# Optimization experiments

Hardware: AMD Instinct MI355X
Metric: run time of the kernel (lower is better)

Reference implementation:

```python
import jax, jax.numpy as jnp
import numpy as np
import math

HIDDEN = 2048
N_HEADS = 16
HEAD_DIM = HIDDEN // N_HEADS
BASE = 10000.0


def setup_inputs() -> dict:
    key = jax.random.key(0)
    ks = jax.random.split(key, 8)
    s = 1.0 / math.sqrt(HIDDEN)
    inp = {
        "hidden_states": jax.random.normal(ks[0], (2, 2048, HIDDEN), dtype=jnp.float32),
        "Wq": jax.random.normal(ks[1], (HIDDEN, HIDDEN), dtype=jnp.float32) * s,
        "bq": jax.random.normal(ks[2], (HIDDEN,), dtype=jnp.float32) * s,
        "Wk": jax.random.normal(ks[3], (HIDDEN, HIDDEN), dtype=jnp.float32) * s,
        "bk": jax.random.normal(ks[4], (HIDDEN,), dtype=jnp.float32) * s,
        "Wv": jax.random.normal(ks[5], (HIDDEN, HIDDEN), dtype=jnp.float32) * s,
        "bv": jax.random.normal(ks[6], (HIDDEN,), dtype=jnp.float32) * s,
        "Wo": jax.random.normal(ks[7], (HIDDEN, HIDDEN), dtype=jnp.float32) * s,
    }
    return inp


def _rotate_half(x):
    x1, x2 = x[..., : x.shape[-1] // 2], x[..., x.shape[-1] // 2 :]
    return jnp.concatenate((-x2, x1), axis=-1)


def _rope_cos_sin(seq_len, dtype):
    inv_freq = 1.0 / (BASE ** (jnp.arange(0, HEAD_DIM, 2, dtype=jnp.float32) / HEAD_DIM))
    t = jnp.arange(seq_len, dtype=jnp.float32)
    freqs = jnp.einsum("i,j->ij", t, inv_freq)  # [S, head_dim/2]
    emb = jnp.concatenate((freqs, freqs), axis=-1)  # [S, head_dim]
    return jnp.cos(emb).astype(dtype), jnp.sin(emb).astype(dtype)


def reference(hidden_states, Wq, bq, Wk, bk, Wv, bv, Wo):
    B, S, _ = hidden_states.shape
    q = hidden_states @ Wq + bq
    k = hidden_states @ Wk + bk
    v = hidden_states @ Wv + bv
    # [B, H, S, D]
    q = q.reshape(B, S, N_HEADS, HEAD_DIM).transpose(0, 2, 1, 3)
    k = k.reshape(B, S, N_HEADS, HEAD_DIM).transpose(0, 2, 1, 3)
    v = v.reshape(B, S, N_HEADS, HEAD_DIM).transpose(0, 2, 1, 3)
    cos, sin = _rope_cos_sin(S, q.dtype)  # [S, D]
    cos = cos[None, None]
    sin = sin[None, None]
    q = q * cos + _rotate_half(q) * sin
    k = k * cos + _rotate_half(k) * sin
    scale = 1.0 / math.sqrt(HEAD_DIM)
    scores = jnp.einsum("bhqd,bhkd->bhqk", q, k) * scale
    attn = jax.nn.softmax(scores, axis=-1)
    out = jnp.einsum("bhqk,bhkd->bhqd", attn, v)
    out = out.transpose(0, 2, 1, 3).reshape(B, S, HIDDEN)
    return out @ Wo
```

## Files before the change

kernel.cpp:

```cpp
#include <hip/hip_runtime.h>

#define HID 2048
#define SEQ 2048
#define HD 128
#define QKN 6144

typedef float f32x4 __attribute__((ext_vector_type(4)));
typedef float f32x16 __attribute__((ext_vector_type(16)));
typedef short s16x8 __attribute__((ext_vector_type(8)));
typedef __bf16 bf16x8 __attribute__((ext_vector_type(8)));

static __device__ __forceinline__ unsigned short f2bf(float x) {
    unsigned u = __float_as_uint(x);
    u = u + 0x7FFFu + ((u >> 16) & 1u);
    return (unsigned short)(u >> 16);
}
static __device__ __forceinline__ float bf2f(unsigned short h) {
    return __uint_as_float(((unsigned)h) << 16);
}
static __device__ __forceinline__ bf16x8 as_bf(s16x8 v) {
    union { s16x8 s; bf16x8 b; } u; u.s = v; return u.b;
}
static __device__ __forceinline__ bf16x8 ld_bf8(const unsigned short* p) {
    return as_bf(*(const s16x8*)p);
}
static __device__ __forceinline__ void gload_lds16(const void* g, void* l) {
    __builtin_amdgcn_global_load_lds(
        (const __attribute__((address_space(1))) void*)g,
        (__attribute__((address_space(3))) void*)l,
        16, 0, 0);
}

__global__ __launch_bounds__(256) void fill_f32(
    float* __restrict__ out, float v, int n)
{
    int i = blockIdx.x * 256 + threadIdx.x;
    if (i < n) out[i] = v;
}

__global__ __launch_bounds__(256) void convert_f32_bf16(
    const float* __restrict__ in, unsigned short* __restrict__ out)
{
    long i = ((long)blockIdx.x * 256 + threadIdx.x) * 8;
    f32x4 a = *(const f32x4*)&in[i];
    f32x4 b = *(const f32x4*)&in[i + 4];
    s16x8 o;
#pragma unroll
    for (int e = 0; e < 4; ++e) {
        o[e]     = (short)f2bf(a[e]);
        o[e + 4] = (short)f2bf(b[e]);
    }
    *(s16x8*)&out[i] = o;
}

__global__ __launch_bounds__(256) void transpose_w4(
    const float* __restrict__ Wq, const float* __restrict__ Wk,
    const float* __restrict__ Wv, const float* __restrict__ Wo,
    unsigned short* __restrict__ wqkvT, unsigned short* __restrict__ woT)
{
    __shared__ float t[32][33];
    const int z = blockIdx.z;
    const float* W = (z == 0) ? Wq : (z == 1) ? Wk : (z == 2) ? Wv : Wo;
    unsigned short* Wt = (z < 3) ? (wqkvT + (long)z * HID * HID) : woT;
    int k0 = blockIdx.x * 32, n0 = blockIdx.y * 32;
    int tx = threadIdx.x & 31, ty = threadIdx.x >> 5;
#pragma unroll
    for (int r = ty; r < 32; r += 8)
        t[r][tx] = W[(long)(k0 + r) * HID + n0 + tx];
    __syncthreads();
#pragma unroll
    for (int r = ty; r < 32; r += 8)
        Wt[(long)(n0 + r) * HID + k0 + tx] = f2bf(t[tx][r]);
}

template<int NF, bool F32OUT, bool ROPE>
__global__ __launch_bounds__(512, 2) void gemm_8phase(
    const unsigned short* __restrict__ A,
    const unsigned short* __restrict__ Bt,
    const float* __restrict__ bq, const float* __restrict__ bk,
    const float* __restrict__ bv,
    unsigned short* __restrict__ Cb, float* __restrict__ Cf,
    int K, int ldc, int nbn, int sm, int sn, int hasBias)
{
    constexpr int BUFE = 16384 + NF * 4096;
    __shared__ unsigned short lds[2 * BUFE];
    const int tid = threadIdx.x;
    const int wid = tid >> 6, lane = tid & 63;
    const int l16 = lane & 15, l4 = lane >> 4;
    const int wm = wid >> 2, wn = wid & 3;

    const int bid = blockIdx.x;
    const int xcd = bid & 7, idx = bid >> 3;
    const int ncn = nbn / sn;
    const int cm = xcd / ncn, cn = xcd % ncn;
    const int lm = idx / sn,  ln = idx % sn;
    const long bm = (long)(cm * sm + lm) * 256;
    const long bn = (long)(cn * sn + ln) * (NF * 64);

    const int NT = K >> 6;
    const long strideB = (long)K * 2;
    const int srow = tid >> 3;
    const int scb  = ((tid & 7) * 16) ^ ((srow & 7) << 4);

    auto stageA = [&](int t, int c) {
        unsigned short* base = &lds[(t & 1) * BUFE];
        const int row = c * 64 + srow;
        const char* src = (const char*)A + (bm + row) * strideB + (long)t * 128 + scb;
        gload_lds16(src, base + (c * 64 + wid * 8) * 64);
    };
    auto stageB = [&](int t, int c) {
        unsigned short* base = &lds[(t & 1) * BUFE + 16384];
        const int row = c * 64 + srow;
        const char* src = (const char*)Bt + (bn + row) * strideB + (long)t * 128 + scb;
        gload_lds16(src, base + (c * 64 + wid * 8) * 64);
    };

    f32x4 acc[8][NF];
#pragma unroll
    for (int i = 0; i < 8; ++i)
#pragma unroll
        for (int j = 0; j < NF; ++j) acc[i][j] = f32x4{0.f, 0.f, 0.f, 0.f};

    auto compute = [&](const unsigned short* Ab, const unsigned short* Bb) {
#pragma unroll
        for (int kk = 0; kk < 2; ++kk) {
            bf16x8 bfr[NF];
#pragma unroll
            for (int j = 0; j < NF; ++j) {
                const int row = wn * (NF * 16) + j * 16 + l16;
                const char* rb = (const char*)Bb + row * 128;
                bfr[j] = as_bf(*(const s16x8*)(rb + ((kk * 64 + l4 * 16) ^ ((l16 & 7) << 4))));
            }
#pragma unroll
            for (int half = 0; half < 2; ++half) {
                bf16x8 af[4];
#pragma unroll
                for (int i = 0; i < 4; ++i) {
                    const int row = wm * 128 + (half * 4 + i) * 16 + l16;
                    const char* rb = (const char*)Ab + row * 128;
                    af[i] = as_bf(*(const s16x8*)(rb + ((kk * 64 + l4 * 16) ^ ((l16 & 7) << 4))));
                }
                __builtin_amdgcn_s_setprio(1);
#pragma unroll
                for (int i = 0; i < 4; ++i)
#pragma unroll
                    for (int j = 0; j < NF; ++j)
                        acc[half * 4 + i][j] = __builtin_amdgcn_mfma_f32_16x16x32_bf16(
                            af[i], bfr[j], acc[half * 4 + i][j], 0, 0, 0);
                __builtin_amdgcn_s_setprio(0);
            }
        }
    };

#pragma unroll
    for (int c = 0; c < 4; ++c) stageA(0, c);
#pragma unroll
    for (int c = 0; c < NF; ++c) stageB(0, c);

    for (int t = 0; t < NT - 1; ++t) {
        const unsigned short* Ab = &lds[(t & 1) * BUFE];
        const unsigned short* Bb = Ab + 16384;
#pragma unroll
        for (int c = 0; c < 4; ++c) stageA(t + 1, c);
#pragma unroll
        for (int c = 0; c < NF; ++c) stageB(t + 1, c);
        __builtin_amdgcn_sched_barrier(0);
        if constexpr (NF == 6)      asm volatile("s_waitcnt vmcnt(10)" ::: "memory");
        else if constexpr (NF == 3) asm volatile("s_waitcnt vmcnt(7)" ::: "memory");
        else                        asm volatile("s_waitcnt vmcnt(6)" ::: "memory");
        __builtin_amdgcn_s_barrier();
        __builtin_amdgcn_sched_barrier(0);
        compute(Ab, Bb);
        __builtin_amdgcn_s_barrier();
    }
    {
        const unsigned short* Ab = &lds[((NT - 1) & 1) * BUFE];
        const unsigned short* Bb = Ab + 16384;
        asm volatile("s_waitcnt vmcnt(0)" ::: "memory");
        __builtin_amdgcn_s_barrier();
        __builtin_amdgcn_sched_barrier(0);
        compute(Ab, Bb);
    }

    float bvv[NF];
#pragma unroll
    for (int nf = 0; nf < NF; ++nf) {
        const long n = bn + wn * (NF * 16) + nf * 16 + l16;
        bvv[nf] = 0.f;
        if (hasBias)
            bvv[nf] = (n < HID) ? bq[n] : ((n < 2 * HID) ? bk[n - HID] : bv[n - 2 * HID]);
    }

    if constexpr (ROPE) {
        constexpr int NH = NF / 2;
        float* fl = (float*)lds;
        const int jr = tid & 63;
        const int rquo = tid >> 6;
        const float inv = exp2f(-(float)jr * 0.20762050593046f);
#pragma unroll
        for (int c = 0; c < 4; ++c) {
            __builtin_amdgcn_s_barrier();
            if (wm == (c >> 1)) {
                const int mf0 = (c & 1) * 4;
#pragma unroll
                for (int mfi = 0; mfi < 4; ++mfi)
#pragma unroll
                    for (int r = 0; r < 4; ++r) {
                        const int rl = mfi * 16 + l4 * 4 + r;
#pragma unroll
                        for (int nf = 0; nf < NF; ++nf)
                            fl[rl * 385 + wn * (NF * 16) + nf * 16 + l16] =
                                acc[mf0 + mfi][nf][r] + bvv[nf];
                    }
            }
            __builtin_amdgcn_s_barrier();
#pragma unroll
            for (int rr = 0; rr < 8; ++rr) {
                const int rl = rr * 8 + rquo;
                const long m = bm + (c >> 1) * 128 + (c & 1) * 64 + rl;
                const int s = (int)(m & (SEQ - 1));
                float sn, cs;
                sincosf((float)s * inv, &sn, &cs);
#pragma unroll
                for (int hh = 0; hh < NH; ++hh) {
                    const long n = bn + hh * 128 + jr;
                    const bool ron = n < 2 * HID;
                    const float qsv = (n < HID) ? 0.12751744581845f : 1.0f;
                    const float se = ron ? sn : 0.f;
                    const float ce = ron ? cs : 1.f;
                    const float x1 = fl[rl * 385 + hh * 128 + jr];
                    const float x2 = fl[rl * 385 + hh * 128 + jr + 64];
                    Cb[m * (long)ldc + n]      = f2bf((x1 * ce - x2 * se) * qsv);
                    Cb[m * (long)ldc + n + 64] = f2bf((x2 * ce + x1 * se) * qsv);
                }
            }
        }
    } else {
#pragma unroll
        for (int mf = 0; mf < 8; ++mf) {
#pragma unroll
            for (int r = 0; r < 4; ++r) {
                const long m = bm + wm * 128 + mf * 16 + l4 * 4 + r;
#pragma unroll
                for (int nf = 0; nf < NF; ++nf) {
                    const long n = bn + wn * (NF * 16) + nf * 16 + l16;
                    float v = acc[mf][nf][r] + bvv[nf];
                    if (F32OUT) Cf[m * (long)ldc + n] = v;
                    else        Cb[m * (long)ldc + n] = f2bf(v);
                }
            }
        }
    }
}

__global__ __launch_bounds__(256) void v_transpose(
    const unsigned short* __restrict__ qkv, unsigned short* __restrict__ vt)
{
    __shared__ unsigned short t[32][33];
    int bh = blockIdx.z;
    int b = bh >> 4, h = bh & 15;
    int s0 = blockIdx.x * 32, d0 = blockIdx.y * 32;
    int tx = threadIdx.x & 31, ty = threadIdx.x >> 5;
#pragma unroll
    for (int r = ty; r < 32; r += 8)
        t[r][tx] = qkv[(long)(b * SEQ + s0 + r) * QKN + 2 * HID + h * HD + d0 + tx];
    __syncthreads();
#pragma unroll
    for (int r = ty; r < 32; r += 8)
        vt[((long)bh * HD + d0 + r) * SEQ + s0 + tx] = t[tx][r];
}

__global__ __launch_bounds__(512, 2) void attn_kernel(
    const unsigned short* __restrict__ qkv,
    const unsigned short* __restrict__ vt,
    unsigned short* __restrict__ attnout)
{
    __shared__ unsigned short Ks[2][64 * 128];
    __shared__ unsigned short Vs[2][128 * 64];

    const int tid = threadIdx.x, wid = tid >> 6, lane = tid & 63;
    const int l32 = lane & 31, hh = lane >> 5;
    const int l16 = lane & 15, l4 = lane >> 4;
    const int bid = blockIdx.x;
    const int xcd = bid & 7, idx = bid >> 3;
    const int bh = xcd * 4 + (idx >> 3);
    const int qt = idx & 7;
    const int b = bh >> 4, h = bh & 15;
    const long rowbase = (long)b * SEQ;

    const unsigned short* Kg = &qkv[rowbase * QKN + HID + h * HD];
    const unsigned short* Vg = &vt[(long)bh * HD * SEQ];

    auto stage = [&](int buf, int kv0) {
#pragma unroll
        for (int i = 0; i < 2; ++i) {
            int c = wid * 2 + i;
            int kr = c * 4 + l4;
            int kcb = (l16 * 16) ^ ((kr & 7) << 4);
            gload_lds16((const char*)(Kg + (long)(kv0 + kr) * QKN) + kcb, &Ks[buf][c * 512]);
            int vr = c * 8 + (lane >> 3);
            int vcb = ((lane & 7) * 16) ^ ((vr & 7) << 4);
            gload_lds16((const char*)(Vg + (long)vr * SEQ + kv0) + vcb, &Vs[buf][c * 512]);
        }
    };

    bf16x8 qf[8];
    {
        const long qrow = rowbase + qt * 256 + wid * 32 + l32;
        const unsigned short* qp = &qkv[qrow * QKN + h * HD];
#pragma unroll
        for (int ks = 0; ks < 8; ++ks)
            qf[ks] = ld_bf8(qp + ks * 16 + hh * 8);
    }

    f32x16 ob[4];
#pragma unroll
    for (int db = 0; db < 4; ++db)
#pragma unroll
        for (int r = 0; r < 16; ++r) ob[db][r] = 0.f;
    float mrun = -3.0e38f, lrun = 0.f;

    stage(0, 0);
    __syncthreads();

    for (int t = 0; t < SEQ / 64; ++t) {
        const int cur = t & 1;
        if (t < SEQ / 64 - 1) stage(cur ^ 1, (t + 1) * 64);
        __builtin_amdgcn_sched_barrier(0);

        const unsigned short* Kc = &Ks[cur][0];
        const unsigned short* Vc = &Vs[cur][0];

        f32x16 sc[2];
#pragma unroll
        for (int kb = 0; kb < 2; ++kb)
#pragma unroll
            for (int r = 0; r < 16; ++r) sc[kb][r] = 0.f;
#pragma unroll
        for (int ks = 0; ks < 8; ++ks) {
#pragma unroll
            for (int kb = 0; kb < 2; ++kb) {
                int row = kb * 32 + l32;
                int cb = (ks * 32 + hh * 16) ^ ((row & 7) << 4);
                bf16x8 kf = as_bf(*(const s16x8*)((const char*)Kc + row * 256 + cb));
                sc[kb] = __builtin_amdgcn_mfma_f32_32x32x16_bf16(kf, qf[ks], sc[kb], 0, 0, 0);
            }
        }

        float tmax = sc[0][0];
#pragma unroll
        for (int kb = 0; kb < 2; ++kb)
#pragma unroll
            for (int r = 0; r < 16; ++r) tmax = fmaxf(tmax, sc[kb][r]);
        tmax = fmaxf(tmax, __shfl_xor(tmax, 32, 64));

        if (!__all(tmax - mrun <= 8.0f)) {
            float mn = fmaxf(mrun, tmax);
            float e_ = exp2f(mrun - mn);
            mrun = mn;
            lrun *= e_;
            float sr[16];
#pragma unroll
            for (int r = 0; r < 16; ++r)
                sr[r] = __shfl(e_, (r & 3) + 8 * (r >> 2) + 4 * hh, 64);
#pragma unroll
            for (int db = 0; db < 4; ++db)
#pragma unroll
                for (int r = 0; r < 16; ++r) ob[db][r] *= sr[r];
        }

        unsigned pk[2][8];
        float sum = 0.f;
#pragma unroll
        for (int kb = 0; kb < 2; ++kb) {
#pragma unroll
            for (int g = 0; g < 8; ++g) {
                float p0 = exp2f(sc[kb][2 * g]     - mrun);
                float p1 = exp2f(sc[kb][2 * g + 1] - mrun);
                sum += p0 + p1;
                union { __bf16 b[2]; unsigned u; } w;
                w.b[0] = (__bf16)p0; w.b[1] = (__bf16)p1;
                pk[kb][g] = w.u;
            }
        }
        sum += __shfl_xor(sum, 32, 64);
        lrun += sum;

        union { unsigned u[4]; bf16x8 v; } pa[4];
#pragma unroll
        for (int ks = 0; ks < 4; ++ks) {
            const int kb = ks >> 1, base = (ks & 1) * 4;
            unsigned a0 = __shfl_xor(pk[kb][base + 0], 32, 64);
            unsigned a1 = __shfl_xor(pk[kb][base + 1], 32, 64);
            unsigned a2 = __shfl_xor(pk[kb][base + 2], 32, 64);
            unsigned a3 = __shfl_xor(pk[kb][base + 3], 32, 64);
            pa[ks].u[0] = hh ? a2 : pk[kb][base + 0];
            pa[ks].u[1] = hh ? a3 : pk[kb][base + 1];
            pa[ks].u[2] = hh ? pk[kb][base + 2] : a0;
            pa[ks].u[3] = hh ? pk[kb][base + 3] : a1;
        }

#pragma unroll
        for (int ks = 0; ks < 4; ++ks) {
#pragma unroll
            for (int db = 0; db < 4; ++db) {
                int row = db * 32 + l32;
                int cb = (ks * 32 + hh * 16) ^ ((row & 7) << 4);
                bf16x8 vb = as_bf(*(const s16x8*)((const char*)Vc + row * 128 + cb));
                ob[db] = __builtin_amdgcn_mfma_f32_32x32x16_bf16(pa[ks].v, vb, ob[db], 0, 0, 0);
            }
        }
        __syncthreads();
    }

    float linv = 1.f / lrun;
    float li[16];
#pragma unroll
    for (int r = 0; r < 16; ++r)
        li[r] = __shfl(linv, (r & 3) + 8 * (r >> 2) + 4 * hh, 64);
#pragma unroll
    for (int db = 0; db < 4; ++db) {
#pragma unroll
        for (int r = 0; r < 16; ++r) {
            const long m = rowbase + qt * 256 + wid * 32 + (r & 3) + 8 * (r >> 2) + 4 * hh;
            attnout[m * HID + h * HD + db * 32 + l32] = f2bf(ob[db][r] * li[r]);
        }
    }
}

extern "C" void kernel_launch(void* const* d_in, const int* in_sizes, int n_in,
                              void* d_out, int out_size, void* d_ws, size_t ws_size,
                              hipStream_t stream)
{
    const float* hs = (const float*)d_in[0];
    const float* Wq = (const float*)d_in[1];
    const float* bq = (const float*)d_in[2];
    const float* Wk = (const float*)d_in[3];
    const float* bk = (const float*)d_in[4];
    const float* Wv = (const float*)d_in[5];
    const float* bv = (const float*)d_in[6];
    const float* Wo = (const float*)d_in[7];
    float* out = (float*)d_out;

    bool shapes_ok =
        (n_in == 8) && (out_size == 8388608) &&
        in_sizes[0] == 8388608 && in_sizes[1] == 4194304 && in_sizes[2] == 2048 &&
        in_sizes[3] == 4194304 && in_sizes[4] == 2048 && in_sizes[5] == 4194304 &&
        in_sizes[6] == 2048 && in_sizes[7] == 4194304;
    if (!shapes_ok || ws_size < 117440512ull) {
        fill_f32<<<32768, 256, 0, stream>>>(out, shapes_ok ? 1000.f : 0.f, out_size);
        return;
    }

    char* ws = (char*)d_ws;
    unsigned short* hsB     = (unsigned short*)(ws);
    unsigned short* qkvB    = (unsigned short*)(ws + 16777216);
    unsigned short* wqkvT   = (unsigned short*)(ws + 67108864);
    unsigned short* vtB     = (unsigned short*)(ws + 92274688);
    unsigned short* woT     = (unsigned short*)(ws + 109051904);
    unsigned short* attnout = hsB;

    convert_f32_bf16<<<4096, 256, 0, stream>>>(hs, hsB);
    transpose_w4<<<dim3(64, 64, 4), 256, 0, stream>>>(Wq, Wk, Wv, Wo, wqkvT, woT);

    gemm_8phase<6, false, true><<<dim3(256), 512, 0, stream>>>(
        hsB, wqkvT, bq, bk, bv, qkvB, nullptr, 2048, QKN, 16, 8, 4, 1);
    v_transpose<<<dim3(64, 4, 32), 256, 0, stream>>>(qkvB, vtB);
    attn_kernel<<<dim3(256), 512, 0, stream>>>(qkvB, vtB, attnout);
    gemm_8phase<2, true, false><<<dim3(256), 512, 0, stream>>>(
        attnout, woT, nullptr, nullptr, nullptr, nullptr, out, 2048, HID, 16, 4, 8, 0);
}
```

Before: 285.0 us.

## Fuse V transpose into QKV GEMM epilogue and drop standalone transpose kernel

The QKV GEMM epilogue now writes the V columns directly in transposed [b,h,d,s] layout from the LDS staging tile. It skips writing V to the row-major qkv buffer, which removes the separate v_transpose kernel launch and its read and write of the V slice. In exchange, the epilogue does strided packed 32-bit stores along the sequence dimension. Those stores may coalesce less well than the old row-major writes.

```diff
diff --git a/kernel.cpp b/kernel.cpp
--- a/kernel.cpp
+++ b/kernel.cpp
@@ -80,6 +80,7 @@
     const float* __restrict__ bq, const float* __restrict__ bk,
     const float* __restrict__ bv,
     unsigned short* __restrict__ Cb, float* __restrict__ Cf,
+    unsigned short* __restrict__ Vt,
     int K, int ldc, int nbn, int sm, int sn, int hasBias)
 {
     constexpr int BUFE = 16384 + NF * 4096;
@@ -196,6 +197,8 @@
         float* fl = (float*)lds;
         const int jr = tid & 63;
         const int rquo = tid >> 6;
+        const int sp = (tid & 31) * 2;
+        const int dg = tid >> 5;
         const float inv = exp2f(-(float)jr * 0.20762050593046f);
 #pragma unroll
         for (int c = 0; c < 4; ++c) {
@@ -214,24 +217,40 @@
                     }
             }
             __builtin_amdgcn_s_barrier();
+            const long mrow0 = bm + (c >> 1) * 128 + (c & 1) * 64;
 #pragma unroll
             for (int rr = 0; rr < 8; ++rr) {
                 const int rl = rr * 8 + rquo;
-                const long m = bm + (c >> 1) * 128 + (c & 1) * 64 + rl;
+                const long m = mrow0 + rl;
                 const int s = (int)(m & (SEQ - 1));
                 float sn, cs;
                 sincosf((float)s * inv, &sn, &cs);
 #pragma unroll
                 for (int hh = 0; hh < NH; ++hh) {
-                    const long n = bn + hh * 128 + jr;
-                    const bool ron = n < 2 * HID;
-                    const float qsv = (n < HID) ? 0.12751744581845f : 1.0f;
-                    const float se = ron ? sn : 0.f;
-                    const float ce = ron ? cs : 1.f;
+                    const long n0 = bn + hh * 128;
+                    if (n0 >= 2 * HID) continue;
+                    const long n = n0 + jr;
+                    const float qsv = (n0 < HID) ? 0.12751744581845f : 1.0f;
                     const float x1 = fl[rl * 385 + hh * 128 + jr];
                     const float x2 = fl[rl * 385 + hh * 128 + jr + 64];
-                    Cb[m * (long)ldc + n]      = f2bf((x1 * ce - x2 * se) * qsv);
-                    Cb[m * (long)ldc + n + 64] = f2bf((x2 * ce + x1 * se) * qsv);
+                    Cb[m * (long)ldc + n]      = f2bf((x1 * cs - x2 * sn) * qsv);
+                    Cb[m * (long)ldc + n + 64] = f2bf((x2 * cs + x1 * sn) * qsv);
+                }
+            }
+#pragma unroll
+            for (int hh = 0; hh < NH; ++hh) {
+                const long n0 = bn + hh * 128;
+                if (n0 < 2 * HID) continue;
+                const int bb = (int)(mrow0 >> 11);
+                const int sg = (int)(mrow0 & (SEQ - 1)) + sp;
+                const long bh2 = (long)bb * 16 + (int)((n0 - 2 * HID) >> 7);
+#pragma unroll
+                for (int db = 0; db < 8; ++db) {
+                    const int d = db * 16 + dg;
+                    union { unsigned short s2[2]; unsigned u; } w;
+                    w.s2[0] = f2bf(fl[sp       * 385 + hh * 128 + d]);
+                    w.s2[1] = f2bf(fl[(sp + 1) * 385 + hh * 128 + d]);
+                    *(unsigned*)&Vt[(bh2 * HD + d) * SEQ + sg] = w.u;
                 }
             }
         }
@@ -251,23 +270,6 @@
             }
         }
     }
-}
-
-__global__ __launch_bounds__(256) void v_transpose(
-    const unsigned short* __restrict__ qkv, unsigned short* __restrict__ vt)
-{
-    __shared__ unsigned short t[32][33];
-    int bh = blockIdx.z;
-    int b = bh >> 4, h = bh & 15;
-    int s0 = blockIdx.x * 32, d0 = blockIdx.y * 32;
-    int tx = threadIdx.x & 31, ty = threadIdx.x >> 5;
-#pragma unroll
-    for (int r = ty; r < 32; r += 8)
-        t[r][tx] = qkv[(long)(b * SEQ + s0 + r) * QKN + 2 * HID + h * HD + d0 + tx];
-    __syncthreads();
-#pragma unroll
-    for (int r = ty; r < 32; r += 8)
-        vt[((long)bh * HD + d0 + r) * SEQ + s0 + tx] = t[tx][r];
 }
 
 __global__ __launch_bounds__(512, 2) void attn_kernel(
@@ -464,9 +466,8 @@
     transpose_w4<<<dim3(64, 64, 4), 256, 0, stream>>>(Wq, Wk, Wv, Wo, wqkvT, woT);
 
     gemm_8phase<6, false, true><<<dim3(256), 512, 0, stream>>>(
-        hsB, wqkvT, bq, bk, bv, qkvB, nullptr, 2048, QKN, 16, 8, 4, 1);
-    v_transpose<<<dim3(64, 4, 32), 256, 0, stream>>>(qkvB, vtB);
+        hsB, wqkvT, bq, bk, bv, qkvB, nullptr, vtB, 2048, QKN, 16, 8, 4, 1);
     attn_kernel<<<dim3(256), 512, 0, stream>>>(qkvB, vtB, attnout);
     gemm_8phase<2, true, false><<<dim3(256), 512, 0, stream>>>(
-        attnout, woT, nullptr, nullptr, nullptr, nullptr, out, 2048, HID, 16, 4, 8, 0);
-}
+        attnout, woT, nullptr, nullptr, nullptr, nullptr, out, nullptr, 2048, HID, 16, 4, 8, 0);
+}
```

Result: no change. 287.2 us (+0.8%).
